# Kernel optimization log

Hardware: AMD Instinct MI355X
Metric: run time of the kernel (lower is better)

The kernel has to match this reference:

```python
import jax, jax.numpy as jnp
import numpy as np


def dense_image_warp(image, flow):
    """Faithful port of tfa.image.dense_image_warp.
    query(y,x) = grid(y,x) - flow(y,x); bilinear sample with floor clipped to
    [0, size-2] and alpha clipped to [0,1] (matches tfa _interpolate_bilinear 'ij').
    image: [B,H,W,C] float, flow: [B,H,W,2] float -> [B,H,W,C]
    """
    B, H, W, C = image.shape
    gy = jnp.arange(H, dtype=flow.dtype)
    gx = jnp.arange(W, dtype=flow.dtype)
    grid = jnp.stack(jnp.meshgrid(gy, gx, indexing='ij'), axis=-1)  # [H,W,2]
    query = grid[None] - flow  # [B,H,W,2]
    qy, qx = query[..., 0], query[..., 1]
    fy = jnp.clip(jnp.floor(qy), 0.0, H - 2)
    fx = jnp.clip(jnp.floor(qx), 0.0, W - 2)
    ay = jnp.clip(qy - fy, 0.0, 1.0)[..., None]  # [B,H,W,1]
    ax = jnp.clip(qx - fx, 0.0, 1.0)[..., None]
    y0 = fy.astype(jnp.int32)
    x0 = fx.astype(jnp.int32)
    b = jnp.arange(B)[:, None, None]
    tl = image[b, y0, x0]
    tr = image[b, y0, x0 + 1]
    bl = image[b, y0 + 1, x0]
    br = image[b, y0 + 1, x0 + 1]
    top = tl + ax * (tr - tl)
    bot = bl + ax * (br - bl)
    return top + ay * (bot - top)


def setup_inputs() -> dict:
    key = jax.random.key(0)
    ks = jax.random.split(key, 6)
    B, H, W, C = 16, 512, 512, 3
    return {
        'frame_0': jax.random.uniform(ks[0], (B, H, W, C), jnp.float32),
        'frame_1': jax.random.uniform(ks[1], (B, H, W, C), jnp.float32),
        'f_01': jax.random.normal(ks[2], (B, H, W, 2), jnp.float32) * 5.0,
        'f_10': jax.random.normal(ks[3], (B, H, W, 2), jnp.float32) * 5.0,
        'f_t0': jax.random.normal(ks[4], (B, H, W, 2), jnp.float32) * 5.0,
        'f_t1': jax.random.normal(ks[5], (B, H, W, 2), jnp.float32) * 5.0,
    }


def reference(frame_0, frame_1, f_01, f_10, f_t0, f_t1):
    return (
        dense_image_warp(frame_1, f_01),
        dense_image_warp(frame_0, f_10),
        dense_image_warp(frame_0, f_t0),
        dense_image_warp(frame_1, f_t1),
    )
```

## Files before the change

### kernel.cpp

```cpp
#include <hip/hip_runtime.h>

#define HH 512
#define WW 512
#define NPIX (16 * HH * WW)
#define IMG_DW (HH * WW * 3)
#define ROWD_G (WW * 3)

#define TSX   32
#define TSY   32
#define APRX  12
#define APRY  12
#define LWX   (TSX + 2 * APRX)
#define LWY   (TSY + 2 * APRY)
#define LSTR  (LWX * 3)
#define LDSDW (LWY * LSTR)
#define NCHUNK (LDSDW / 4)
#define NTHR  512

typedef float fv4 __attribute__((ext_vector_type(4)));
typedef float fv2 __attribute__((ext_vector_type(2)));
typedef fv4 fv4u __attribute__((aligned(4)));
typedef fv2 fv2u __attribute__((aligned(4)));

__device__ __forceinline__ void sample(const float* __restrict__ imgb,
                                       const float* __restrict__ s,
                                       int AX0, int AY0,
                                       float qy, float qx, float* __restrict__ r)
{
    float fy = floorf(qy); fy = fminf(fmaxf(fy, 0.0f), (float)(HH - 2));
    float fx = floorf(qx); fx = fminf(fmaxf(fx, 0.0f), (float)(WW - 2));
    const float ay = fminf(fmaxf(qy - fy, 0.0f), 1.0f);
    const float ax = fminf(fmaxf(qx - fx, 0.0f), 1.0f);
    const int y0 = (int)fy, x0 = (int)fx;
    const int yl = y0 - AY0, xl = x0 - AX0;
    if ((unsigned)yl < (unsigned)(LWY - 1) && (unsigned)xl < (unsigned)(LWX - 1)) {
        const float* t  = s + yl * LSTR + 3 * xl;
        const float* bo = t + LSTR;
#pragma unroll
        for (int c = 0; c < 3; ++c) {
            const float tl = t[c],  tr = t[c + 3];
            const float bl = bo[c], br = bo[c + 3];
            const float top = tl + ax * (tr - tl);
            const float bot = bl + ax * (br - bl);
            r[c] = top + ay * (bot - top);
        }
    } else {
        const float* t  = imgb + ((size_t)y0 * WW + x0) * 3;
        const float* bo = t + WW * 3;
        const fv4u t4 = *(const fv4u*)t;  const fv2u t2 = *(const fv2u*)(t + 4);
        const fv4u b4 = *(const fv4u*)bo; const fv2u b2 = *(const fv2u*)(bo + 4);
        const float tv[6] = {t4.x, t4.y, t4.z, t4.w, t2.x, t2.y};
        const float bv[6] = {b4.x, b4.y, b4.z, b4.w, b2.x, b2.y};
#pragma unroll
        for (int c = 0; c < 3; ++c) {
            const float top = tv[c] + ax * (tv[c + 3] - tv[c]);
            const float bot = bv[c] + ax * (bv[c + 3] - bv[c]);
            r[c] = top + ay * (bot - top);
        }
    }
}

__global__ __launch_bounds__(NTHR) void warp_wc_kernel(
    const float* __restrict__ frame0, const float* __restrict__ frame1,
    const float* __restrict__ f01, const float* __restrict__ f10,
    const float* __restrict__ ft0, const float* __restrict__ ft1,
    float* __restrict__ out)
{
    __shared__ float lds[LDSDW];

    const unsigned bid = blockIdx.x;
    const unsigned v   = (bid & 7u) * 1024u + (bid >> 3);

    const unsigned tile  = v & 255u;
    const unsigned img_b = v >> 8;
    const int b  = (int)(img_b & 15u);
    const int fg = (int)(img_b >> 4);

    const int tx = (int)(tile & 15u);
    const int ty = (int)(tile >> 4);
    const int X0 = tx * TSX, Y0 = ty * TSY;
    const int AX0 = X0 - APRX, AY0 = Y0 - APRY;

    const float* img   = fg ? frame1 : frame0;
    const float* flowA = fg ? f01 : f10;
    const float* flowB = fg ? ft1 : ft0;
    const size_t opA   = fg ? 0 : 1;
    const size_t opB   = fg ? 3 : 2;

    const float* imgb = img + (size_t)b * IMG_DW;

    const int tid = (int)threadIdx.x;
    const int lx = (tid & 15) * 2;
    const int ly = tid >> 4;
    const int x = X0 + lx, y = Y0 + ly;
    const size_t pixIn = ((size_t)b * HH + y) * WW + x;

    const fv4 a = __builtin_nontemporal_load((const fv4*)(flowA + pixIn * 2));
    const fv4 c = __builtin_nontemporal_load((const fv4*)(flowB + pixIn * 2));

    {
        const unsigned wid = __builtin_amdgcn_readfirstlane((unsigned)tid >> 6);
        int D   = tid * 4;
        int row = D / LSTR;
        int rd  = D - row * LSTR;
#pragma unroll
        for (int it = 0; it < 5; ++it) {
            if (it < 4 || tid < (NCHUNK - 4 * NTHR)) {
                const int gy = min(max(AY0 + row, 0), HH - 1);
                int idx = gy * ROWD_G + AX0 * 3 + rd;
                idx = min(max(idx, 0), IMG_DW - 4);
                const float* src = imgb + idx;
                float* dst = (float*)lds + it * (NTHR * 4) + wid * 256;
                __builtin_amdgcn_global_load_lds(
                    (const __attribute__((address_space(1))) void*)src,
                    (__attribute__((address_space(3))) void*)dst, 16, 0, 0);
            }
            row += 12; rd += 32;
            if (rd >= LSTR) { rd -= LSTR; ++row; }
        }
    }

    float qy0 = (float)y - a.x, qx0 = (float)x       - a.y;
    float qy1 = (float)y - a.z, qx1 = (float)(x + 1) - a.w;
    float qy2 = (float)y - c.x, qx2 = (float)x       - c.y;
    float qy3 = (float)y - c.z, qx3 = (float)(x + 1) - c.w;

    __syncthreads();

    float* oA = out + (opA * NPIX + pixIn) * 3;
    float* oB = out + (opB * NPIX + pixIn) * 3;

    {
        float res[6];
        sample(imgb, lds, AX0, AY0, qy0, qx0, res);
        sample(imgb, lds, AX0, AY0, qy1, qx1, res + 3);
        *(fv2*)oA       = fv2{res[0], res[1]};
        *((fv2*)oA + 1) = fv2{res[2], res[3]};
        *((fv2*)oA + 2) = fv2{res[4], res[5]};
    }
    {
        float res[6];
        sample(imgb, lds, AX0, AY0, qy2, qx2, res);
        sample(imgb, lds, AX0, AY0, qy3, qx3, res + 3);
        *(fv2*)oB       = fv2{res[0], res[1]};
        *((fv2*)oB + 1) = fv2{res[2], res[3]};
        *((fv2*)oB + 2) = fv2{res[4], res[5]};
    }
}

extern "C" void kernel_launch(void* const* d_in, const int* in_sizes, int n_in,
                              void* d_out, int out_size, void* d_ws, size_t ws_size,
                              hipStream_t stream) {
    const float* frame0 = (const float*)d_in[0];
    const float* frame1 = (const float*)d_in[1];
    const float* f01    = (const float*)d_in[2];
    const float* f10    = (const float*)d_in[3];
    const float* ft0    = (const float*)d_in[4];
    const float* ft1    = (const float*)d_in[5];
    float* out = (float*)d_out;

    hipLaunchKernelGGL(warp_wc_kernel, dim3(8192), dim3(NTHR), 0, stream,
                       frame0, frame1, f01, f10, ft0, ft1, out);
}
```

Measured before the change: 94.51 us.

## Widen tiles to 64x32 with four pixels per thread and streaming stores

Tile width is doubled to 64 columns, so each thread handles four adjacent pixels per flow pair and the grid is halved. The LDS halo overhead per output pixel drops because the 12-pixel apron is amortised over a wider tile. Output is now written as 16-byte nontemporal vector stores instead of 8-byte stores. The costs are a larger LDS footprint per block (88x56x3 floats, about 59 KB), which may limit blocks per CU, and more registers per thread.

```diff
diff --git a/kernel.cpp b/kernel.cpp
--- a/kernel.cpp
+++ b/kernel.cpp
@@ -6,7 +6,7 @@
 #define IMG_DW (HH * WW * 3)
 #define ROWD_G (WW * 3)
 
-#define TSX   32
+#define TSX   64
 #define TSY   32
 #define APRX  12
 #define APRY  12
@@ -60,7 +60,7 @@
     }
 }
 
-__global__ __launch_bounds__(NTHR) void warp_wc_kernel(
+__global__ __launch_bounds__(NTHR) void warp_t64_kernel(
     const float* __restrict__ frame0, const float* __restrict__ frame1,
     const float* __restrict__ f01, const float* __restrict__ f10,
     const float* __restrict__ ft0, const float* __restrict__ ft1,
@@ -69,15 +69,15 @@
     __shared__ float lds[LDSDW];
 
     const unsigned bid = blockIdx.x;
-    const unsigned v   = (bid & 7u) * 1024u + (bid >> 3);
+    const unsigned v   = (bid & 7u) * 512u + (bid >> 3);
 
-    const unsigned tile  = v & 255u;
-    const unsigned img_b = v >> 8;
+    const unsigned tile  = v & 127u;
+    const unsigned img_b = v >> 7;
     const int b  = (int)(img_b & 15u);
     const int fg = (int)(img_b >> 4);
 
-    const int tx = (int)(tile & 15u);
-    const int ty = (int)(tile >> 4);
+    const int tx = (int)(tile & 7u);
+    const int ty = (int)(tile >> 3);
     const int X0 = tx * TSX, Y0 = ty * TSY;
     const int AX0 = X0 - APRX, AY0 = Y0 - APRY;
 
@@ -90,13 +90,15 @@
     const float* imgb = img + (size_t)b * IMG_DW;
 
     const int tid = (int)threadIdx.x;
-    const int lx = (tid & 15) * 2;
+    const int lx = (tid & 15) * 4;
     const int ly = tid >> 4;
     const int x = X0 + lx, y = Y0 + ly;
     const size_t pixIn = ((size_t)b * HH + y) * WW + x;
 
-    const fv4 a = __builtin_nontemporal_load((const fv4*)(flowA + pixIn * 2));
-    const fv4 c = __builtin_nontemporal_load((const fv4*)(flowB + pixIn * 2));
+    const fv4 a0 = __builtin_nontemporal_load((const fv4*)(flowA + pixIn * 2));
+    const fv4 a1 = __builtin_nontemporal_load((const fv4*)(flowA + pixIn * 2) + 1);
+    const fv4 c0 = __builtin_nontemporal_load((const fv4*)(flowB + pixIn * 2));
+    const fv4 c1 = __builtin_nontemporal_load((const fv4*)(flowB + pixIn * 2) + 1);
 
     {
         const unsigned wid = __builtin_amdgcn_readfirstlane((unsigned)tid >> 6);
@@ -104,8 +106,8 @@
         int row = D / LSTR;
         int rd  = D - row * LSTR;
 #pragma unroll
-        for (int it = 0; it < 5; ++it) {
-            if (it < 4 || tid < (NCHUNK - 4 * NTHR)) {
+        for (int it = 0; it < 8; ++it) {
+            if (it < 7 || tid < (NCHUNK - 7 * NTHR)) {
                 const int gy = min(max(AY0 + row, 0), HH - 1);
                 int idx = gy * ROWD_G + AX0 * 3 + rd;
                 idx = min(max(idx, 0), IMG_DW - 4);
@@ -115,15 +117,15 @@
                     (const __attribute__((address_space(1))) void*)src,
                     (__attribute__((address_space(3))) void*)dst, 16, 0, 0);
             }
-            row += 12; rd += 32;
+            row += 7; rd += 200;
             if (rd >= LSTR) { rd -= LSTR; ++row; }
         }
     }
 
-    float qy0 = (float)y - a.x, qx0 = (float)x       - a.y;
-    float qy1 = (float)y - a.z, qx1 = (float)(x + 1) - a.w;
-    float qy2 = (float)y - c.x, qx2 = (float)x       - c.y;
-    float qy3 = (float)y - c.z, qx3 = (float)(x + 1) - c.w;
+    const float flyA[4] = {a0.x, a0.z, a1.x, a1.z};
+    const float flxA[4] = {a0.y, a0.w, a1.y, a1.w};
+    const float flyB[4] = {c0.x, c0.z, c1.x, c1.z};
+    const float flxB[4] = {c0.y, c0.w, c1.y, c1.w};
 
     __syncthreads();
 
@@ -131,20 +133,28 @@
     float* oB = out + (opB * NPIX + pixIn) * 3;
 
     {
-        float res[6];
-        sample(imgb, lds, AX0, AY0, qy0, qx0, res);
-        sample(imgb, lds, AX0, AY0, qy1, qx1, res + 3);
-        *(fv2*)oA       = fv2{res[0], res[1]};
-        *((fv2*)oA + 1) = fv2{res[2], res[3]};
-        *((fv2*)oA + 2) = fv2{res[4], res[5]};
+        float res[12];
+#pragma unroll
+        for (int p = 0; p < 4; ++p)
+            sample(imgb, lds, AX0, AY0, (float)y - flyA[p], (float)(x + p) - flxA[p], res + 3 * p);
+        fv4 s0 = {res[0], res[1], res[2],  res[3]};
+        fv4 s1 = {res[4], res[5], res[6],  res[7]};
+        fv4 s2 = {res[8], res[9], res[10], res[11]};
+        __builtin_nontemporal_store(s0, (fv4*)oA);
+        __builtin_nontemporal_store(s1, (fv4*)oA + 1);
+        __builtin_nontemporal_store(s2, (fv4*)oA + 2);
     }
     {
-        float res[6];
-        sample(imgb, lds, AX0, AY0, qy2, qx2, res);
-        sample(imgb, lds, AX0, AY0, qy3, qx3, res + 3);
-        *(fv2*)oB       = fv2{res[0], res[1]};
-        *((fv2*)oB + 1) = fv2{res[2], res[3]};
-        *((fv2*)oB + 2) = fv2{res[4], res[5]};
+        float res[12];
+#pragma unroll
+        for (int p = 0; p < 4; ++p)
+            sample(imgb, lds, AX0, AY0, (float)y - flyB[p], (float)(x + p) - flxB[p], res + 3 * p);
+        fv4 s0 = {res[0], res[1], res[2],  res[3]};
+        fv4 s1 = {res[4], res[5], res[6],  res[7]};
+        fv4 s2 = {res[8], res[9], res[10], res[11]};
+        __builtin_nontemporal_store(s0, (fv4*)oB);
+        __builtin_nontemporal_store(s1, (fv4*)oB + 1);
+        __builtin_nontemporal_store(s2, (fv4*)oB + 2);
     }
 }
 
@@ -159,6 +169,6 @@
     const float* ft1    = (const float*)d_in[5];
     float* out = (float*)d_out;
 
-    hipLaunchKernelGGL(warp_wc_kernel, dim3(8192), dim3(NTHR), 0, stream,
+    hipLaunchKernelGGL(warp_t64_kernel, dim3(4096), dim3(NTHR), 0, stream,
                        frame0, frame1, f01, f10, ft0, ft1, out);
 }
```

Measured after the change: 103.7 us. +9.8%, slower.
